# Kernel optimization log

Hardware: AMD Instinct MI355X
Metric: run time of the kernel (lower is better)

## Reference

```python
import jax, jax.numpy as jnp
import numpy as np

SIZE_DICT = 512
DIM_DICT = 256
TEMPERATURE = 0.5
EPS = 1e-10


def setup_inputs() -> dict:
    key = jax.random.key(0)
    k1, k2, k3 = jax.random.split(key, 3)
    bs, dim_z, W, H = 32, DIM_DICT, 32, 32
    z_from_encoder = jax.random.normal(k1, (bs, dim_z, W, H), dtype=jnp.float32)
    kappa_q = jnp.ones((1,), dtype=jnp.float32)
    codebook = jax.random.normal(k2, (SIZE_DICT, DIM_DICT), dtype=jnp.float32)
    gumbel_u = jax.random.uniform(k3, (bs * W * H, SIZE_DICT), dtype=jnp.float32)
    return {"z_from_encoder": z_from_encoder, "kappa_q": kappa_q,
            "codebook": codebook, "gumbel_u": gumbel_u, "flg_train": 1}


def reference(z_from_encoder, kappa_q, codebook, gumbel_u, flg_train):
    bs, dim_z, W, H = z_from_encoder.shape
    # [bs, dim_z, W, H] -> [bs*W*H, dim_z]
    z_flat = jnp.transpose(z_from_encoder, (0, 2, 3, 1)).reshape(-1, dim_z)
    kq = jnp.clip(kappa_q, 1e-5, 1e5)  # scalar-ish [1]
    # L2-normalize codebook rows
    cb = codebook / jnp.linalg.norm(codebook, axis=1, keepdims=True)
    # logit = -distance = kappa * <z, c>   [N, K]
    logit = kq * (z_flat @ cb.T)
    logit = logit - jnp.max(logit, axis=-1, keepdims=True)
    logit = jnp.clip(logit, -50.0, 50.0)
    probabilities = jax.nn.softmax(logit, axis=-1)
    log_probabilities = jax.nn.log_softmax(logit, axis=-1)
    # training path: gumbel-softmax relaxation
    g = -jnp.log(-jnp.log(gumbel_u + EPS) + EPS)
    encodings = jax.nn.softmax((logit + g) / TEMPERATURE, axis=-1)
    z_quantized = (encodings @ cb).reshape(bs, W, H, dim_z)
    avg_probs = jnp.mean(jax.lax.stop_gradient(probabilities), axis=0)
    z_to_decoder = jnp.transpose(z_quantized, (0, 3, 1, 2))
    kld_discrete = jnp.sum(probabilities * log_probabilities) / bs
    kld_continuous = jnp.mean(
        jnp.sum(z_from_encoder * (z_from_encoder - z_to_decoder) * kq[0],
                axis=(1, 2, 3)))
    loss = kld_discrete + kld_continuous
    avg_probs = jnp.clip(avg_probs, 1e-10, None)
    perplexity = jnp.exp(-jnp.sum(avg_probs * jnp.log(avg_probs + 1e-10)))
    return z_to_decoder, loss, perplexity
```

## Files before the change

kernel.cpp:

```cpp
#include <hip/hip_runtime.h>
#include <stdint.h>


typedef float v4f __attribute__((ext_vector_type(4)));
typedef short v8s __attribute__((ext_vector_type(8)));
typedef short v4s __attribute__((ext_vector_type(4)));

#define ZA_STR 264
#define L2_STR 520

__device__ __forceinline__ uint16_t f2bf(float x) {
  uint32_t u = __float_as_uint(x);
  u = u + 0x7fffu + ((u >> 16) & 1u);
  return (uint16_t)(u >> 16);
}
__device__ __forceinline__ float bf2f(uint16_t h) {
  return __uint_as_float(((uint32_t)h) << 16);
}


__global__ __launch_bounds__(64) void vq_prep0(const float* __restrict__ cb,
                                               char* __restrict__ ws) {
  const int blk = blockIdx.x, t = threadIdx.x;
  float* shadow = (float*)(ws + 524288);
  float* scal   = (float*)(ws + 557056);
  float* rnorm  = (float*)(ws + 557072);
  if (blk < 512) {
    float s = 0.f;
#pragma unroll
    for (int i = 0; i < 4; i++) { const float v = cb[blk * 256 + t + 64 * i]; s += v * v; }
#pragma unroll
    for (int mm = 1; mm < 64; mm <<= 1) s += __shfl_xor(s, mm, 64);
    if (t == 0) rnorm[blk] = 1.0f / sqrtf(s);
  } else if (blk < 528) {
    const int j = blk - 512;
#pragma unroll
    for (int i = 0; i < 8; i++) shadow[j * 512 + t + 64 * i] = 0.f;
  } else {
    if (t < 3) scal[t] = 0.f;
  }
}

__global__ __launch_bounds__(256) void vq_prep1(const float* __restrict__ cb,
                                                char* __restrict__ ws) {
  const int b = blockIdx.x, t = threadIdx.x;
  uint16_t* cbn2 = (uint16_t*)ws;
  uint16_t* cbt2 = (uint16_t*)(ws + 262144);
  const float* rnorm = (const float*)(ws + 557072);
  union { v8s v; uint16_t u[8]; } pk;
  if (b < 64) {
    const int g = b * 256 + t;
    const int code = g >> 5, dch = g & 31;
    const float rn = rnorm[code];
    const float4 f0 = *(const float4*)(cb + code * 256 + dch * 8);
    const float4 f1 = *(const float4*)(cb + code * 256 + dch * 8 + 4);
    pk.u[0] = f2bf(f0.x * rn); pk.u[1] = f2bf(f0.y * rn);
    pk.u[2] = f2bf(f0.z * rn); pk.u[3] = f2bf(f0.w * rn);
    pk.u[4] = f2bf(f1.x * rn); pk.u[5] = f2bf(f1.y * rn);
    pk.u[6] = f2bf(f1.z * rn); pk.u[7] = f2bf(f1.w * rn);
    const int w = code >> 7, ct = (code >> 4) & 7, mcol = code & 15;
    const int ks = dch >> 2, q3 = dch & 3;
    *(v8s*)(cbn2 + ((ks * 8 + ct) * 4 + w) * 512 + (q3 * 16 + mcol) * 8) = pk.v;
  } else {
    const int g = (b - 64) * 256 + t;
    const int cgroup = g >> 8, d = g & 255;
#pragma unroll
    for (int j = 0; j < 8; j++) {
      const int c = cgroup * 8 + j;
      pk.u[j] = f2bf(cb[c * 256 + d] * rnorm[c]);
    }
    const int cc = cgroup >> 2, qq = cgroup & 3;
    const int wd = d >> 6, nt = (d >> 4) & 3, md = d & 15;
    *(v8s*)(cbt2 + ((cc * 4 + nt) * 4 + wd) * 512 + (qq * 16 + md) * 8) = pk.v;
  }
}

__global__ __launch_bounds__(256, 4) void vq_main(const float* __restrict__ z,
                                                  const float* __restrict__ kappa,
                                                  const float* __restrict__ gum,
                                                  char* __restrict__ ws,
                                                  float* __restrict__ out) {
  __shared__ char s_A[33280];
  __shared__ float s_pm[128], s_pS[128], s_pT[128];
  __shared__ float s_M[32], s_rS[32], s_kd[32], s_rSe[32], s_red[8];

  const int t = threadIdx.x;
  const int w = t >> 6, lane = t & 63, q = lane >> 4, m = lane & 15;
  const int bi = blockIdx.x, b = bi >> 5, wh0 = (bi & 31) << 5;
  const int R0 = bi << 5;

  const uint16_t* cbn2 = (const uint16_t*)ws;
  const uint16_t* cbt2 = (const uint16_t*)(ws + 262144);
  float* shadow = (float*)(ws + 524288);
  float* scal   = (float*)(ws + 557056);

  uint16_t* za  = (uint16_t*)s_A;
  uint16_t* l2s = (uint16_t*)s_A;

  const float kq = fminf(fmaxf(kappa[0], 1e-5f), 1e5f);

  const int row = t >> 3, c4 = (t & 7) << 2;
  const float* gbase = gum + (size_t)(R0 + row) * 512 + c4;

  {
    float zs = 0.f;
    const int whb = (t & 7) << 2, dT = t >> 3;
    const float* zb = z + ((size_t)b << 18) + wh0 + whb;
#pragma unroll
    for (int s = 0; s < 8; s++) {
      const int d = dT + (s << 5);
      const float4 v = *(const float4*)(zb + (d << 10));
      zs += v.x * v.x + v.y * v.y + v.z * v.z + v.w * v.w;
      za[(whb + 0) * ZA_STR + d] = f2bf(v.x);
      za[(whb + 1) * ZA_STR + d] = f2bf(v.y);
      za[(whb + 2) * ZA_STR + d] = f2bf(v.z);
      za[(whb + 3) * ZA_STR + d] = f2bf(v.w);
    }
#pragma unroll
    for (int mm = 1; mm < 64; mm <<= 1) zs += __shfl_xor(zs, mm, 64);
    if (lane == 0) s_red[w] = zs;
  }

  float4 gq[4];
#pragma unroll
  for (int i = 0; i < 4; i++) gq[i] = *(const float4*)(gbase + (i << 5));

  __syncthreads();
  if (t == 0) atomicAdd(&scal[1], s_red[0] + s_red[1] + s_red[2] + s_red[3]);

  v4f acc0[8], acc1[8];
#pragma unroll
  for (int i = 0; i < 8; i++) { acc0[i] = (v4f)0.f; acc1[i] = (v4f)0.f; }
  {
    const uint16_t* bp  = cbn2 + (w << 9) + (lane << 3);
    const uint16_t* a0p = za + m * ZA_STR;
    const uint16_t* a1p = za + (m + 16) * ZA_STR;
#pragma unroll
    for (int ks = 0; ks < 8; ks++) {
      const v8s a0 = *(const v8s*)(a0p + (ks << 5) + (q << 3));
      const v8s a1 = *(const v8s*)(a1p + (ks << 5) + (q << 3));
#pragma unroll
      for (int ct = 0; ct < 8; ct++) {
        const v8s bf = *(const v8s*)(bp + (((ks << 3) + ct) << 11));
        acc0[ct] = __builtin_amdgcn_mfma_f32_16x16x32_bf16(a0, bf, acc0[ct], 0, 0, 0);
        acc1[ct] = __builtin_amdgcn_mfma_f32_16x16x32_bf16(a1, bf, acc1[ct], 0, 0, 0);
      }
    }
  }
#pragma unroll
  for (int i = 0; i < 8; i++) { acc0[i] *= kq; acc1[i] *= kq; }

  {
    auto stats_half = [&](v4f (&acc)[8], int half) {
#pragma unroll
      for (int reg = 0; reg < 4; reg++) {
        float mx = -1e30f;
#pragma unroll
        for (int ct = 0; ct < 8; ct++) mx = fmaxf(mx, acc[ct][reg]);
#pragma unroll
        for (int mm = 1; mm < 16; mm <<= 1) mx = fmaxf(mx, __shfl_xor(mx, mm, 64));
        float S = 0.f, T = 0.f;
#pragma unroll
        for (int ct = 0; ct < 8; ct++) {
          const float d = acc[ct][reg] - mx;
          const float e = __expf(d);
          S += e; T += d * e;
        }
#pragma unroll
        for (int mm = 1; mm < 16; mm <<= 1) { S += __shfl_xor(S, mm, 64); T += __shfl_xor(T, mm, 64); }
        if (m == 0) {
          const int r = half * 16 + q * 4 + reg;
          s_pm[(w << 5) + r] = mx; s_pS[(w << 5) + r] = S; s_pT[(w << 5) + r] = T;
        }
      }
    };
    stats_half(acc0, 0);
    stats_half(acc1, 1);
  }
  __syncthreads();
  if (t < 32) {
    float M = s_pm[t];
    M = fmaxf(M, s_pm[32 + t]); M = fmaxf(M, s_pm[64 + t]); M = fmaxf(M, s_pm[96 + t]);
    float S = 0.f, T = 0.f;
#pragma unroll
    for (int ww = 0; ww < 4; ww++) {
      const float dm = s_pm[ww * 32 + t] - M;
      const float al = __expf(dm);
      S += s_pS[ww * 32 + t] * al;
      T += (s_pT[ww * 32 + t] + dm * s_pS[ww * 32 + t]) * al;
    }
    const float rS = 1.0f / S;
    s_M[t] = M; s_rS[t] = rS; s_kd[t] = T * rS - __logf(S);
  }
  __syncthreads();

  {
    const int c0 = w << 7;
    float colacc[8];
#pragma unroll
    for (int i = 0; i < 8; i++) colacc[i] = 0.f;
    auto pass2_half = [&](v4f (&acc)[8], int half) {
#pragma unroll
      for (int reg = 0; reg < 4; reg++) {
        const int r = half * 16 + q * 4 + reg;
        const float Mr = s_M[r], rSr = s_rS[r];
        uint16_t* lrow = l2s + r * L2_STR + c0 + m;
#pragma unroll
        for (int ct = 0; ct < 8; ct++) {
          const float d = fmaxf(acc[ct][reg] - Mr, -50.0f);
          const float e = __expf(d);
          colacc[ct] += e * rSr;
          lrow[ct << 4] = f2bf(e);
        }
      }
    };
    pass2_half(acc0, 0);
    pass2_half(acc1, 1);
#pragma unroll
    for (int i = 0; i < 8; i++) {
      colacc[i] += __shfl_xor(colacc[i], 16, 64);
      colacc[i] += __shfl_xor(colacc[i], 32, 64);
    }
    if (q == 0) {
      float* sh = shadow + ((bi & 15) << 9) + c0 + m;
#pragma unroll
      for (int i = 0; i < 8; i++) atomicAdd(&sh[i << 4], colacc[i]);
    }
    if (w == 0) {
      float kd = s_kd[lane & 31];
#pragma unroll
      for (int mm = 1; mm < 64; mm <<= 1) kd += __shfl_xor(kd, mm, 64);
      if (lane == 0) atomicAdd(&scal[0], 0.5f * kd);
    }
  }
  __syncthreads();

  {
    const float mxr = s_M[row];
    float se = 0.f, ce = 0.f;
    union { v4s v; uint16_t h[4]; } ev, rv;
#pragma unroll
    for (int i = 0; i < 16; i++) {
      const float4 u = gq[i & 3];
      const float uu[4] = {u.x, u.y, u.z, u.w};
      ev.v = *(const v4s*)(l2s + row * L2_STR + (i << 5) + c4);
      if (i < 12) gq[i & 3] = *(const float4*)(gbase + ((i + 4) << 5));
#pragma unroll
      for (int j = 0; j < 4; j++) {
        const float e = bf2f(ev.h[j]);
        const float L = -__logf(uu[j] + 1e-10f) + 1e-10f;
        const float f = __fdividef(e, L);
        const float er = f * f;
        se += er;
        ce += er * (__logf(e) + mxr);
        rv.h[j] = f2bf(er);
      }
      *(v4s*)(l2s + row * L2_STR + (i << 5) + c4) = rv.v;
    }
#pragma unroll
    for (int mm = 1; mm < 8; mm <<= 1) { se += __shfl_xor(se, mm, 64); ce += __shfl_xor(ce, mm, 64); }
    float cr = ((t & 7) == 0) ? (ce / se) : 0.f;
#pragma unroll
    for (int mm = 8; mm < 64; mm <<= 1) cr += __shfl_xor(cr, mm, 64);
    if (lane == 0) s_red[w] = cr;
    if ((t & 7) == 0) s_rSe[row] = 1.0f / se;
  }
  __syncthreads();
  if (t == 0) atomicAdd(&scal[2], s_red[0] + s_red[1] + s_red[2] + s_red[3]);

  v4f acc2a[4], acc2b[4];
#pragma unroll
  for (int i = 0; i < 4; i++) { acc2a[i] = (v4f)0.f; acc2b[i] = (v4f)0.f; }
  {
    const uint16_t* a0p = l2s + m * L2_STR;
    const uint16_t* a1p = l2s + (m + 16) * L2_STR;
#pragma unroll
    for (int cc = 0; cc < 16; cc++) {
      const v8s a0 = *(const v8s*)(a0p + (cc << 5) + (q << 3));
      const v8s a1 = *(const v8s*)(a1p + (cc << 5) + (q << 3));
      const uint16_t* bp2 = cbt2 + (cc << 13) + (w << 9) + (lane << 3);
#pragma unroll
      for (int nt = 0; nt < 4; nt++) {
        const v8s bf = *(const v8s*)(bp2 + (nt << 11));
        acc2a[nt] = __builtin_amdgcn_mfma_f32_16x16x32_bf16(a0, bf, acc2a[nt], 0, 0, 0);
        acc2b[nt] = __builtin_amdgcn_mfma_f32_16x16x32_bf16(a1, bf, acc2b[nt], 0, 0, 0);
      }
    }
  }

  {
    float* ob = out + ((size_t)b << 18) + wh0;
    const int d0 = w << 6;
    float rsA[4], rsB[4];
#pragma unroll
    for (int reg = 0; reg < 4; reg++) {
      rsA[reg] = s_rSe[q * 4 + reg];
      rsB[reg] = s_rSe[16 + q * 4 + reg];
    }
#pragma unroll
    for (int nt = 0; nt < 4; nt++) {
      const int d = d0 + (nt << 4) + m;
#pragma unroll
      for (int reg = 0; reg < 4; reg++) {
        ob[(d << 10) + q * 4 + reg]      = acc2a[nt][reg] * rsA[reg];
        ob[(d << 10) + 16 + q * 4 + reg] = acc2b[nt][reg] * rsB[reg];
      }
    }
  }
}

__global__ __launch_bounds__(512) void vq_final(const float* __restrict__ kappa,
                                                char* __restrict__ ws,
                                                float* __restrict__ out) {
  __shared__ float red[8];
  const int t = threadIdx.x;
  const float* shadow = (const float*)(ws + 524288);
  const float* scal   = (const float*)(ws + 557056);
  float s = 0.f;
#pragma unroll
  for (int j = 0; j < 16; j++) s += shadow[(j << 9) + t];
  float avg = fmaxf(s * (1.0f / 32768.0f), 1e-10f);
  float term = avg * __logf(avg + 1e-10f);
#pragma unroll
  for (int mm = 1; mm < 64; mm <<= 1) term += __shfl_xor(term, mm, 64);
  if ((t & 63) == 0) red[t >> 6] = term;
  __syncthreads();
  if (t == 0) {
    float H = 0.f;
#pragma unroll
    for (int i = 0; i < 8; i++) H += red[i];
    const float perpl = __expf(-H);
    const float kq = fminf(fmaxf(kappa[0], 1e-5f), 1e5f);
    const float loss = (scal[0] + kq * scal[1] - scal[2]) * (1.0f / 32.0f);
    out[8388608] = loss;
    out[8388609] = perpl;
  }
}

extern "C" void kernel_launch(void* const* d_in, const int* in_sizes, int n_in,
                              void* d_out, int out_size, void* d_ws, size_t ws_size,
                              hipStream_t stream) {
  const float* z     = (const float*)d_in[0];
  const float* kappa = (const float*)d_in[1];
  const float* cb    = (const float*)d_in[2];
  const float* gum   = (const float*)d_in[3];
  char* ws = (char*)d_ws;
  float* out = (float*)d_out;
  hipLaunchKernelGGL(vq_prep0, dim3(529),  dim3(64),  0, stream, cb, ws);
  hipLaunchKernelGGL(vq_prep1, dim3(128),  dim3(256), 0, stream, cb, ws);
  hipLaunchKernelGGL(vq_main,  dim3(1024), dim3(256), 0, stream, z, kappa, gum, ws, out);
  hipLaunchKernelGGL(vq_final, dim3(1),    dim3(512), 0, stream, kappa, ws, out);
}
```

Before: 200.6 us.

## Shrink main tile to 16 rows with 2 waves, re-layout codebook tiles

Each main-kernel block now handles 16 rows with 128 threads (2 waves), giving 2048 blocks instead of 1024. Each wave covers 256 codes (16 MFMA column tiles), and the prep kernel re-lays out both codebook copies to match. Shared memory per block is halved and the output is written as float4. The cost is that each codebook B fragment is reused for only 16 rows instead of 32, so global/L2 traffic for codebook reads doubles, and the per-wave register footprint rises.

```diff
diff --git a/kernel.cpp b/kernel.cpp
--- a/kernel.cpp
+++ b/kernel.cpp
@@ -58,9 +58,9 @@
     pk.u[2] = f2bf(f0.z * rn); pk.u[3] = f2bf(f0.w * rn);
     pk.u[4] = f2bf(f1.x * rn); pk.u[5] = f2bf(f1.y * rn);
     pk.u[6] = f2bf(f1.z * rn); pk.u[7] = f2bf(f1.w * rn);
-    const int w = code >> 7, ct = (code >> 4) & 7, mcol = code & 15;
+    const int w2 = code >> 8, ct = (code >> 4) & 15, mcol = code & 15;
     const int ks = dch >> 2, q3 = dch & 3;
-    *(v8s*)(cbn2 + ((ks * 8 + ct) * 4 + w) * 512 + (q3 * 16 + mcol) * 8) = pk.v;
+    *(v8s*)(cbn2 + ((((ks << 4) + ct) * 2 + w2) << 9) + (((q3 << 4) + mcol) << 3)) = pk.v;
   } else {
     const int g = (b - 64) * 256 + t;
     const int cgroup = g >> 8, d = g & 255;
@@ -70,24 +70,24 @@
       pk.u[j] = f2bf(cb[c * 256 + d] * rnorm[c]);
     }
     const int cc = cgroup >> 2, qq = cgroup & 3;
-    const int wd = d >> 6, nt = (d >> 4) & 3, md = d & 15;
-    *(v8s*)(cbt2 + ((cc * 4 + nt) * 4 + wd) * 512 + (qq * 16 + md) * 8) = pk.v;
-  }
-}
-
-__global__ __launch_bounds__(256, 4) void vq_main(const float* __restrict__ z,
+    const int wd = d >> 7, nt = (d >> 4) & 7, md = d & 15;
+    *(v8s*)(cbt2 + ((((cc << 3) + nt) * 2 + wd) << 9) + (((qq << 4) + md) << 3)) = pk.v;
+  }
+}
+
+__global__ __launch_bounds__(128, 4) void vq_main(const float* __restrict__ z,
                                                   const float* __restrict__ kappa,
                                                   const float* __restrict__ gum,
                                                   char* __restrict__ ws,
                                                   float* __restrict__ out) {
-  __shared__ char s_A[33280];
-  __shared__ float s_pm[128], s_pS[128], s_pT[128];
-  __shared__ float s_M[32], s_rS[32], s_kd[32], s_rSe[32], s_red[8];
+  __shared__ char s_A[16640];
+  __shared__ float s_pm[32], s_pS[32], s_pT[32];
+  __shared__ float s_M[16], s_rS[16], s_kd[16], s_rSe[16], s_red[2];
 
   const int t = threadIdx.x;
   const int w = t >> 6, lane = t & 63, q = lane >> 4, m = lane & 15;
-  const int bi = blockIdx.x, b = bi >> 5, wh0 = (bi & 31) << 5;
-  const int R0 = bi << 5;
+  const int bi = blockIdx.x, b = bi >> 6, wh0 = (bi & 63) << 4;
+  const int R0 = bi << 4;
 
   const uint16_t* cbn2 = (const uint16_t*)ws;
   const uint16_t* cbt2 = (const uint16_t*)(ws + 262144);
@@ -104,7 +104,7 @@
 
   {
     float zs = 0.f;
-    const int whb = (t & 7) << 2, dT = t >> 3;
+    const int whb = (t & 3) << 2, dT = t >> 2;
     const float* zb = z + ((size_t)b << 18) + wh0 + whb;
 #pragma unroll
     for (int s = 0; s < 8; s++) {
@@ -126,111 +126,96 @@
   for (int i = 0; i < 4; i++) gq[i] = *(const float4*)(gbase + (i << 5));
 
   __syncthreads();
-  if (t == 0) atomicAdd(&scal[1], s_red[0] + s_red[1] + s_red[2] + s_red[3]);
-
-  v4f acc0[8], acc1[8];
-#pragma unroll
-  for (int i = 0; i < 8; i++) { acc0[i] = (v4f)0.f; acc1[i] = (v4f)0.f; }
-  {
-    const uint16_t* bp  = cbn2 + (w << 9) + (lane << 3);
-    const uint16_t* a0p = za + m * ZA_STR;
-    const uint16_t* a1p = za + (m + 16) * ZA_STR;
+  if (t == 0) atomicAdd(&scal[1], s_red[0] + s_red[1]);
+
+  v4f acc[16];
+#pragma unroll
+  for (int i = 0; i < 16; i++) acc[i] = (v4f)0.f;
+  {
+    const uint16_t* bp = cbn2 + (w << 9) + (lane << 3);
+    const uint16_t* ap = za + m * ZA_STR;
 #pragma unroll
     for (int ks = 0; ks < 8; ks++) {
-      const v8s a0 = *(const v8s*)(a0p + (ks << 5) + (q << 3));
-      const v8s a1 = *(const v8s*)(a1p + (ks << 5) + (q << 3));
-#pragma unroll
-      for (int ct = 0; ct < 8; ct++) {
-        const v8s bf = *(const v8s*)(bp + (((ks << 3) + ct) << 11));
-        acc0[ct] = __builtin_amdgcn_mfma_f32_16x16x32_bf16(a0, bf, acc0[ct], 0, 0, 0);
-        acc1[ct] = __builtin_amdgcn_mfma_f32_16x16x32_bf16(a1, bf, acc1[ct], 0, 0, 0);
-      }
-    }
-  }
-#pragma unroll
-  for (int i = 0; i < 8; i++) { acc0[i] *= kq; acc1[i] *= kq; }
-
-  {
-    auto stats_half = [&](v4f (&acc)[8], int half) {
-#pragma unroll
-      for (int reg = 0; reg < 4; reg++) {
-        float mx = -1e30f;
-#pragma unroll
-        for (int ct = 0; ct < 8; ct++) mx = fmaxf(mx, acc[ct][reg]);
-#pragma unroll
-        for (int mm = 1; mm < 16; mm <<= 1) mx = fmaxf(mx, __shfl_xor(mx, mm, 64));
-        float S = 0.f, T = 0.f;
-#pragma unroll
-        for (int ct = 0; ct < 8; ct++) {
-          const float d = acc[ct][reg] - mx;
-          const float e = __expf(d);
-          S += e; T += d * e;
-        }
-#pragma unroll
-        for (int mm = 1; mm < 16; mm <<= 1) { S += __shfl_xor(S, mm, 64); T += __shfl_xor(T, mm, 64); }
-        if (m == 0) {
-          const int r = half * 16 + q * 4 + reg;
-          s_pm[(w << 5) + r] = mx; s_pS[(w << 5) + r] = S; s_pT[(w << 5) + r] = T;
-        }
-      }
-    };
-    stats_half(acc0, 0);
-    stats_half(acc1, 1);
-  }
-  __syncthreads();
-  if (t < 32) {
-    float M = s_pm[t];
-    M = fmaxf(M, s_pm[32 + t]); M = fmaxf(M, s_pm[64 + t]); M = fmaxf(M, s_pm[96 + t]);
-    float S = 0.f, T = 0.f;
-#pragma unroll
-    for (int ww = 0; ww < 4; ww++) {
-      const float dm = s_pm[ww * 32 + t] - M;
-      const float al = __expf(dm);
-      S += s_pS[ww * 32 + t] * al;
-      T += (s_pT[ww * 32 + t] + dm * s_pS[ww * 32 + t]) * al;
-    }
+      const v8s a = *(const v8s*)(ap + (ks << 5) + (q << 3));
+#pragma unroll
+      for (int ct = 0; ct < 16; ct++) {
+        const v8s bf = *(const v8s*)(bp + (((ks << 4) + ct) << 10));
+        acc[ct] = __builtin_amdgcn_mfma_f32_16x16x32_bf16(a, bf, acc[ct], 0, 0, 0);
+      }
+    }
+  }
+#pragma unroll
+  for (int i = 0; i < 16; i++) acc[i] *= kq;
+
+  {
+#pragma unroll
+    for (int reg = 0; reg < 4; reg++) {
+      float mx = -1e30f;
+#pragma unroll
+      for (int ct = 0; ct < 16; ct++) mx = fmaxf(mx, acc[ct][reg]);
+#pragma unroll
+      for (int mm = 1; mm < 16; mm <<= 1) mx = fmaxf(mx, __shfl_xor(mx, mm, 64));
+      float S = 0.f, T = 0.f;
+#pragma unroll
+      for (int ct = 0; ct < 16; ct++) {
+        const float d = acc[ct][reg] - mx;
+        const float e = __expf(d);
+        S += e; T += d * e;
+      }
+#pragma unroll
+      for (int mm = 1; mm < 16; mm <<= 1) { S += __shfl_xor(S, mm, 64); T += __shfl_xor(T, mm, 64); }
+      if (m == 0) {
+        const int r = q * 4 + reg;
+        s_pm[(w << 4) + r] = mx; s_pS[(w << 4) + r] = S; s_pT[(w << 4) + r] = T;
+      }
+    }
+  }
+  __syncthreads();
+  if (t < 16) {
+    const float m0 = s_pm[t], m1 = s_pm[16 + t];
+    const float M = fmaxf(m0, m1);
+    const float a0 = __expf(m0 - M), a1 = __expf(m1 - M);
+    const float S = s_pS[t] * a0 + s_pS[16 + t] * a1;
+    const float T = (s_pT[t] + (m0 - M) * s_pS[t]) * a0
+                  + (s_pT[16 + t] + (m1 - M) * s_pS[16 + t]) * a1;
     const float rS = 1.0f / S;
     s_M[t] = M; s_rS[t] = rS; s_kd[t] = T * rS - __logf(S);
   }
   __syncthreads();
 
   {
-    const int c0 = w << 7;
-    float colacc[8];
-#pragma unroll
-    for (int i = 0; i < 8; i++) colacc[i] = 0.f;
-    auto pass2_half = [&](v4f (&acc)[8], int half) {
-#pragma unroll
-      for (int reg = 0; reg < 4; reg++) {
-        const int r = half * 16 + q * 4 + reg;
-        const float Mr = s_M[r], rSr = s_rS[r];
-        uint16_t* lrow = l2s + r * L2_STR + c0 + m;
-#pragma unroll
-        for (int ct = 0; ct < 8; ct++) {
-          const float d = fmaxf(acc[ct][reg] - Mr, -50.0f);
-          const float e = __expf(d);
-          colacc[ct] += e * rSr;
-          lrow[ct << 4] = f2bf(e);
-        }
-      }
-    };
-    pass2_half(acc0, 0);
-    pass2_half(acc1, 1);
-#pragma unroll
-    for (int i = 0; i < 8; i++) {
+    const int c0 = w << 8;
+    float colacc[16];
+#pragma unroll
+    for (int i = 0; i < 16; i++) colacc[i] = 0.f;
+#pragma unroll
+    for (int reg = 0; reg < 4; reg++) {
+      const int r = q * 4 + reg;
+      const float Mr = s_M[r], rSr = s_rS[r];
+      uint16_t* lrow = l2s + r * L2_STR + c0 + m;
+#pragma unroll
+      for (int ct = 0; ct < 16; ct++) {
+        const float d = fmaxf(acc[ct][reg] - Mr, -50.0f);
+        const float e = __expf(d);
+        colacc[ct] += e * rSr;
+        lrow[ct << 4] = f2bf(e);
+      }
+    }
+#pragma unroll
+    for (int i = 0; i < 16; i++) {
       colacc[i] += __shfl_xor(colacc[i], 16, 64);
       colacc[i] += __shfl_xor(colacc[i], 32, 64);
     }
     if (q == 0) {
       float* sh = shadow + ((bi & 15) << 9) + c0 + m;
 #pragma unroll
-      for (int i = 0; i < 8; i++) atomicAdd(&sh[i << 4], colacc[i]);
+      for (int i = 0; i < 16; i++) atomicAdd(&sh[i << 4], colacc[i]);
     }
     if (w == 0) {
-      float kd = s_kd[lane & 31];
+      float kd = (lane < 16) ? s_kd[lane] : 0.f;
 #pragma unroll
       for (int mm = 1; mm < 64; mm <<= 1) kd += __shfl_xor(kd, mm, 64);
-      if (lane == 0) atomicAdd(&scal[0], 0.5f * kd);
+      if (lane == 0) atomicAdd(&scal[0], kd);
     }
   }
   __syncthreads();
@@ -266,45 +251,37 @@
     if ((t & 7) == 0) s_rSe[row] = 1.0f / se;
   }
   __syncthreads();
-  if (t == 0) atomicAdd(&scal[2], s_red[0] + s_red[1] + s_red[2] + s_red[3]);
-
-  v4f acc2a[4], acc2b[4];
-#pragma unroll
-  for (int i = 0; i < 4; i++) { acc2a[i] = (v4f)0.f; acc2b[i] = (v4f)0.f; }
-  {
-    const uint16_t* a0p = l2s + m * L2_STR;
-    const uint16_t* a1p = l2s + (m + 16) * L2_STR;
+  if (t == 0) atomicAdd(&scal[2], s_red[0] + s_red[1]);
+
+  v4f acc2[8];
+#pragma unroll
+  for (int i = 0; i < 8; i++) acc2[i] = (v4f)0.f;
+  {
+    const uint16_t* a2p = l2s + m * L2_STR;
+    const uint16_t* bp2 = cbt2 + (w << 9) + (lane << 3);
 #pragma unroll
     for (int cc = 0; cc < 16; cc++) {
-      const v8s a0 = *(const v8s*)(a0p + (cc << 5) + (q << 3));
-      const v8s a1 = *(const v8s*)(a1p + (cc << 5) + (q << 3));
-      const uint16_t* bp2 = cbt2 + (cc << 13) + (w << 9) + (lane << 3);
-#pragma unroll
-      for (int nt = 0; nt < 4; nt++) {
-        const v8s bf = *(const v8s*)(bp2 + (nt << 11));
-        acc2a[nt] = __builtin_amdgcn_mfma_f32_16x16x32_bf16(a0, bf, acc2a[nt], 0, 0, 0);
-        acc2b[nt] = __builtin_amdgcn_mfma_f32_16x16x32_bf16(a1, bf, acc2b[nt], 0, 0, 0);
-      }
-    }
-  }
-
-  {
-    float* ob = out + ((size_t)b << 18) + wh0;
-    const int d0 = w << 6;
-    float rsA[4], rsB[4];
-#pragma unroll
-    for (int reg = 0; reg < 4; reg++) {
-      rsA[reg] = s_rSe[q * 4 + reg];
-      rsB[reg] = s_rSe[16 + q * 4 + reg];
-    }
-#pragma unroll
-    for (int nt = 0; nt < 4; nt++) {
-      const int d = d0 + (nt << 4) + m;
-#pragma unroll
-      for (int reg = 0; reg < 4; reg++) {
-        ob[(d << 10) + q * 4 + reg]      = acc2a[nt][reg] * rsA[reg];
-        ob[(d << 10) + 16 + q * 4 + reg] = acc2b[nt][reg] * rsB[reg];
-      }
+      const v8s a = *(const v8s*)(a2p + (cc << 5) + (q << 3));
+#pragma unroll
+      for (int nt = 0; nt < 8; nt++) {
+        const v8s bf = *(const v8s*)(bp2 + ((((cc << 3) + nt)) << 10));
+        acc2[nt] = __builtin_amdgcn_mfma_f32_16x16x32_bf16(a, bf, acc2[nt], 0, 0, 0);
+      }
+    }
+  }
+
+  {
+    float* ob = out + ((size_t)b << 18) + wh0 + (q << 2);
+    float rs[4];
+#pragma unroll
+    for (int reg = 0; reg < 4; reg++) rs[reg] = s_rSe[(q << 2) + reg];
+#pragma unroll
+    for (int nt = 0; nt < 8; nt++) {
+      const int d = (w << 7) + (nt << 4) + m;
+      float4 v;
+      v.x = acc2[nt][0] * rs[0]; v.y = acc2[nt][1] * rs[1];
+      v.z = acc2[nt][2] * rs[2]; v.w = acc2[nt][3] * rs[3];
+      *(float4*)(ob + (d << 10)) = v;
     }
   }
 }
@@ -348,6 +325,6 @@
   float* out = (float*)d_out;
   hipLaunchKernelGGL(vq_prep0, dim3(529),  dim3(64),  0, stream, cb, ws);
   hipLaunchKernelGGL(vq_prep1, dim3(128),  dim3(256), 0, stream, cb, ws);
-  hipLaunchKernelGGL(vq_main,  dim3(1024), dim3(256), 0, stream, z, kappa, gum, ws, out);
+  hipLaunchKernelGGL(vq_main,  dim3(2048), dim3(128), 0, stream, z, kappa, gum, ws, out);
   hipLaunchKernelGGL(vq_final, dim3(1),    dim3(512), 0, stream, kappa, ws, out);
 }
```

Result: slower. 240.2 us (+19.8%).
